# Performance work log

Hardware: AMD Instinct MI355X
Metric: run time of the kernel (lower is better)

The kernel has to match this reference:

```python
import jax, jax.numpy as jnp
import numpy as np

N_PTS, HID, N_LAYERS, N_HEAD, B = 21, 128, 4, 4, 8192
EPS_LN = 1e-6


def _cheb(x, adj, W, b):
    # ChebConv with K=2 (3 orders): T0=I, T1=L, T2=2*L@L - I, L = I - D^-1/2 A D^-1/2
    d = jnp.sum(adj, axis=-1) ** -0.5
    L = jnp.eye(N_PTS, dtype=x.dtype) - d[:, None] * adj * d[None, :]
    t1 = jnp.einsum('ij,bjc->bic', L, x)
    t2 = 2.0 * jnp.einsum('ij,bjc->bic', L, t1) - x
    return (jnp.einsum('bnc,cd->bnd', x, W[0])
            + jnp.einsum('bnc,cd->bnd', t1, W[1])
            + jnp.einsum('bnc,cd->bnd', t2, W[2])) + b


def _layer_norm(x, a, b):
    # matches custom LayerNorm: unbiased std (torch default), eps added to std
    mean = jnp.mean(x, -1, keepdims=True)
    xm = x - mean
    std = jnp.sqrt(jnp.sum(xm * xm, -1, keepdims=True) / (x.shape[-1] - 1))
    return a * xm / (std + EPS_LN) + b


def _mha(x, mask, Wq, bq, Wk, bk, Wv, bv, Wo, bo):
    Bn, N, D = x.shape
    dk = D // N_HEAD
    def proj(W, b):
        return (x @ W + b).reshape(Bn, N, N_HEAD, dk).transpose(0, 2, 1, 3)
    Q, K, V = proj(Wq, bq), proj(Wk, bk), proj(Wv, bv)
    scores = jnp.einsum('bhqd,bhkd->bhqk', Q, K) / np.float32(np.sqrt(dk))
    scores = jnp.where(mask[:, None, :, :], scores, jnp.asarray(-1e9, x.dtype))
    p = jax.nn.softmax(scores, axis=-1)  # dropout is identity at eval
    o = jnp.einsum('bhqk,bhkd->bhqd', p, V).transpose(0, 2, 1, 3).reshape(Bn, N, D)
    return o @ Wo + bo


def _graphnet(x, Ahat, W1, b1, W2, b2):
    # GraphNet feed-forward: two GraphConvs with learnable A_hat
    # laplacian_batch: D from column sums (torch.sum over dim=1), A_hat same per batch
    d = (jnp.sum(Ahat, axis=0) + 1e-5) ** -0.5
    L = d[:, None] * Ahat * d[None, :]
    h = jax.nn.relu(jnp.einsum('ij,bjc->bic', L, x) @ W1 + b1)
    return jnp.einsum('ij,bjc->bic', L, h) @ W2 + b2


def _forward(x, mask, adj, W_in, b_in, W_out, b_out, ln1_a, ln1_b, ln2_a, ln2_b,
             Wq, bq, Wk, bk, Wv, bv, Wo, bo, Ahat, Wg1, bg1, Wg2, bg2,
             Wc1, bc1, Wc2, bc2):
    out = _cheb(x, adj, W_in, b_in)  # [B,21,128]
    for i in range(N_LAYERS):
        # EncoderLayer: pre-norm residual attn, then pre-norm residual GraphNet
        h = _layer_norm(out, ln1_a[i], ln1_b[i])
        out = out + _mha(h, mask, Wq[i], bq[i], Wk[i], bk[i], Wv[i], bv[i], Wo[i], bo[i])
        h = _layer_norm(out, ln2_a[i], ln2_b[i])
        out = out + _graphnet(h, Ahat[i], Wg1[i], bg1[i], Wg2[i], bg2[i])
        # _ResChebGC: residual + relu(cheb(relu(cheb(x))))
        g = jax.nn.relu(_cheb(out, adj, Wc1[i], bc1[i]))
        out = out + jax.nn.relu(_cheb(g, adj, Wc2[i], bc2[i]))
    return _cheb(out, adj, W_out, b_out)  # [B,21,3]


def setup_inputs() -> dict:
    key = jax.random.key(0)
    ks = iter(jax.random.split(key, 40))
    def nrm(shape, s=0.02):
        return jax.random.normal(next(ks), shape, jnp.float32) * s
    L = N_LAYERS
    return dict(
        x=jax.random.normal(next(ks), (B, N_PTS, 2), jnp.float32),
        mask=jnp.ones((1, 1, N_PTS), dtype=bool),
        adj=jax.random.uniform(next(ks), (N_PTS, N_PTS), jnp.float32) + jnp.eye(N_PTS, dtype=jnp.float32),
        W_in=nrm((3, 2, HID), 0.2), b_in=jnp.zeros((HID,), jnp.float32),
        W_out=nrm((3, HID, 3), 0.05), b_out=jnp.zeros((3,), jnp.float32),
        ln1_a=jnp.ones((L, HID), jnp.float32), ln1_b=jnp.zeros((L, HID), jnp.float32),
        ln2_a=jnp.ones((L, HID), jnp.float32), ln2_b=jnp.zeros((L, HID), jnp.float32),
        Wq=nrm((L, HID, HID)), bq=jnp.zeros((L, HID), jnp.float32),
        Wk=nrm((L, HID, HID)), bk=jnp.zeros((L, HID), jnp.float32),
        Wv=nrm((L, HID, HID)), bv=jnp.zeros((L, HID), jnp.float32),
        Wo=nrm((L, HID, HID)), bo=jnp.zeros((L, HID), jnp.float32),
        Ahat=jnp.tile(jnp.eye(N_PTS, dtype=jnp.float32)[None], (L, 1, 1)),
        Wg1=nrm((L, HID, 2 * HID)), bg1=jnp.zeros((L, 2 * HID), jnp.float32),
        Wg2=nrm((L, 2 * HID, HID)), bg2=jnp.zeros((L, HID), jnp.float32),
        Wc1=nrm((L, 3, HID, HID)), bc1=jnp.zeros((L, HID), jnp.float32),
        Wc2=nrm((L, 3, HID, HID)), bc2=jnp.zeros((L, HID), jnp.float32),
    )


def reference(x, mask, adj, W_in, b_in, W_out, b_out, ln1_a, ln1_b, ln2_a, ln2_b,
              Wq, bq, Wk, bk, Wv, bv, Wo, bo, Ahat, Wg1, bg1, Wg2, bg2,
              Wc1, bc1, Wc2, bc2):
    return _forward(x, mask, adj, W_in, b_in, W_out, b_out, ln1_a, ln1_b, ln2_a, ln2_b,
                    Wq, bq, Wk, bk, Wv, bv, Wo, bo, Ahat, Wg1, bg1, Wg2, bg2,
                    Wc1, bc1, Wc2, bc2)
```

## Files before the change

kernel.cpp:

```cpp
#include <hip/hip_runtime.h>

#define DEV static __device__ __forceinline__

typedef __attribute__((ext_vector_type(8))) short short8;
typedef __attribute__((ext_vector_type(4))) short short4v;
typedef __attribute__((ext_vector_type(4))) float f4;

#define OFF_QKV 0
#define OFF_WO  196608
#define OFF_WG1 262144
#define OFF_WG2 393216
#define OFF_WC1 524288
#define OFF_WC2 720896
#define OFF_WIN 917504
#define OFF_WOUT 929792
#define OFF_M1 931840
#define OFF_M2 932864
#define OFF_LG 933888
#define W_TOT  937984

struct WSBuf {
  unsigned short w[W_TOT];
  float m1f[441];
  float m2f[441];
};
__device__ WSBuf g_ws;

DEV float b2f(unsigned short u){ union { unsigned int i; float f; } v; v.i = ((unsigned int)u)<<16; return v.f; }
DEV unsigned short f2b(float f){
  union { float f; unsigned int i; } v; v.f = f;
  unsigned int i = v.i; i += 0x7fffu + ((i>>16)&1u);
  return (unsigned short)(i>>16);
}
DEV f4 mfma(short8 a, short8 b, f4 c){ return __builtin_amdgcn_mfma_f32_16x16x32_bf16(a,b,c,0,0,0); }
DEV f4 mfma16(short4v a, short4v b, f4 c){ return __builtin_amdgcn_mfma_f32_16x16x16bf16_1k(a,b,c,0,0,0); }
DEV short8 ld8(const unsigned short* p){ return *(const short8*)p; }

DEV void st4(unsigned short* p, f4 v){
  short4v o;
  o[0]=(short)f2b(v[0]); o[1]=(short)f2b(v[1]);
  o[2]=(short)f2b(v[2]); o[3]=(short)f2b(v[3]);
  *(short4v*)p = o;
}
DEV void rmw4(unsigned short* p, f4 v){
  short4v x = *(const short4v*)p;
  short4v o;
  o[0]=(short)f2b(b2f((unsigned short)x[0]) + v[0]);
  o[1]=(short)f2b(b2f((unsigned short)x[1]) + v[1]);
  o[2]=(short)f2b(b2f((unsigned short)x[2]) + v[2]);
  o[3]=(short)f2b(b2f((unsigned short)x[3]) + v[3]);
  *(short4v*)p = o;
}
DEV f4 maxz(f4 v){
  v[0]=fmaxf(v[0],0.f); v[1]=fmaxf(v[1],0.f);
  v[2]=fmaxf(v[2],0.f); v[3]=fmaxf(v[3],0.f);
  return v;
}

__global__ void prep_mats(const float* __restrict__ adj,
                          const float* __restrict__ Ahat){
  __shared__ float sA[441], sL[441], sM2[441], sD[21];
  unsigned short* ws = g_ws.w;
  int t = threadIdx.x;
  if (t < 441) sA[t] = adj[t];
  __syncthreads();
  if (t < 21){ float s = 0.f; for (int j=0;j<21;++j) s += sA[t*21+j]; sD[t] = 1.0f/sqrtf(s); }
  __syncthreads();
  if (t < 441){ int i = t/21, j = t%21; sL[t] = ((i==j)?1.f:0.f) - sD[i]*sA[t]*sD[j]; }
  __syncthreads();
  if (t < 441){ int i = t/21, j = t%21; float a=0.f;
    for (int m=0;m<21;++m) a += sL[i*21+m]*sL[m*21+j];
    sM2[t] = 2.f*a - ((i==j)?1.f:0.f); }
  __syncthreads();
  for (int e = t; e < 1024; e += blockDim.x){
    int i = e>>5, j = e&31; bool v = (i<21)&&(j<21);
    ws[OFF_M1+e] = v ? f2b(sL[i*21+j]) : 0;
    ws[OFF_M2+e] = v ? f2b(sM2[i*21+j]) : 0;
  }
  if (t < 441){ g_ws.m1f[t] = sL[t]; g_ws.m2f[t] = sM2[t]; }
  for (int l=0;l<4;++l){
    __syncthreads();
    if (t < 441) sA[t] = Ahat[l*441 + t];
    __syncthreads();
    if (t < 21){ float s = 1e-5f; for (int i=0;i<21;++i) s += sA[i*21+t]; sD[t] = 1.0f/sqrtf(s); }
    __syncthreads();
    for (int e = t; e < 1024; e += blockDim.x){
      int i = e>>5, j = e&31; bool v = (i<21)&&(j<21);
      ws[OFF_LG + l*1024 + e] = v ? f2b(sD[i]*sA[i*21+j]*sD[j]) : 0;
    }
  }
}

__global__ void prep_tw(const float* __restrict__ Wq, const float* __restrict__ Wk,
                        const float* __restrict__ Wv, const float* __restrict__ Wo,
                        const float* __restrict__ Wg1, const float* __restrict__ Wg2,
                        const float* __restrict__ Wc1, const float* __restrict__ Wc2,
                        const float* __restrict__ Win, const float* __restrict__ Wout){
  unsigned short* ws = g_ws.w;
  int stride = gridDim.x*blockDim.x;
  int idx = blockIdx.x*blockDim.x + threadIdx.x;
  for (int e = idx; e < 196608; e += stride){
    int l = e/49152, r = e%49152, n = r>>7, k = r&127;
    int sel = n>>7, c = n&127;
    const float* W = (sel==0)?Wq:((sel==1)?Wk:Wv);
    ws[OFF_QKV+e] = f2b(W[l*16384 + k*128 + c]);
  }
  for (int e = idx; e < 65536; e += stride){
    int l = e>>14, r = e&16383, n = r>>7, k = r&127;
    ws[OFF_WO+e] = f2b(Wo[l*16384 + k*128 + n]);
  }
  for (int e = idx; e < 131072; e += stride){
    int l = e>>15, r = e&32767, n = r>>7, k = r&127;
    ws[OFF_WG1+e] = f2b(Wg1[l*32768 + k*256 + n]);
  }
  for (int e = idx; e < 131072; e += stride){
    int l = e>>15, r = e&32767, n = r>>8, k = r&255;
    ws[OFF_WG2+e] = f2b(Wg2[l*32768 + k*128 + n]);
  }
  for (int e = idx; e < 196608; e += stride){
    int l = e/49152, r = e%49152, n = r>>7, k = r&127;
    int sel = n>>7, c = n&127;
    ws[OFF_WC1+e] = f2b(Wc1[((l*3+sel)*128 + k)*128 + c]);
  }
  for (int e = idx; e < 196608; e += stride){
    int l = e/49152, r = e%49152, n = r>>7, k = r&127;
    int sel = n>>7, c = n&127;
    ws[OFF_WC2+e] = f2b(Wc2[((l*3+sel)*128 + k)*128 + c]);
  }
  for (int e = idx; e < 12288; e += stride){
    int n = e>>5, k = e&31, sel = n>>7, c = n&127;
    ws[OFF_WIN+e] = (k<2) ? f2b(Win[(sel*2 + k)*128 + c]) : 0;
  }
  for (int e = idx; e < 2048; e += stride){
    int n = e>>7, k = e&127;
    ws[OFF_WOUT+e] = (n<9) ? f2b(Wout[((n/3)*128 + k)*3 + (n%3)]) : 0;
  }
}

#define PA 152

template<int MT, int NT, int KS>
DEV void chan_mm(const unsigned short* A, int pitchA,
                 const unsigned short* Bt, int strideB, int n0, int mt0,
                 int lane, f4 acc[MT][NT]){
  const int l16 = lane & 15, qd = lane >> 4;
#pragma unroll
  for (int ks = 0; ks < KS; ++ks){
    const int k0 = ks*32 + qd*8;
    short8 af[MT];
#pragma unroll
    for (int m=0; m<MT; ++m) af[m] = ld8(A + ((mt0+m)*16+l16)*pitchA + k0);
#pragma unroll
    for (int nt=0; nt<NT; ++nt){
      short8 bf = ld8(Bt + (n0 + nt*16 + l16)*strideB + k0);
#pragma unroll
      for (int m=0; m<MT; ++m) acc[m][nt] = mfma(af[m], bf, acc[m][nt]);
    }
  }
}

DEV void node_mm1(const unsigned short* Ut, int mt0,
                  const unsigned short* Mr, int lane, f4 acc[3][2]){
  const int l16 = lane & 15, qd = lane >> 4;
  short8 bf[2];
#pragma unroll
  for (int nt=0; nt<2; ++nt) bf[nt] = ld8(Mr + (nt*16+l16)*32 + qd*8);
#pragma unroll
  for (int b=0;b<3;++b){
    short8 af = ld8(Ut + (mt0*16 + l16)*72 + b*24 + qd*8);
#pragma unroll
    for (int nt=0;nt<2;++nt) acc[b][nt] = mfma(af, bf[nt], acc[b][nt]);
  }
}

template<int KS>
DEV void w0_term1(const unsigned short* Wt0, int sK,
                  const unsigned short* Blds, int pitchB, int mt0,
                  int lane, f4 acc[3][2]){
  const int l16 = lane&15, qd = lane>>4;
#pragma unroll
  for (int ks=0; ks<KS; ++ks){
    const int k0 = ks*32 + qd*8;
    short8 af = ld8(Wt0 + (mt0*16+l16)*sK + k0);
#pragma unroll
    for (int b=0;b<3;++b){
#pragma unroll
      for (int nt=0;nt<2;++nt){
        short8 bf = ld8(Blds + (b*21 + nt*16 + l16)*pitchB + k0);
        acc[b][nt] = mfma(af, bf, acc[b][nt]);
      }
    }
  }
}

DEV void write_tr(unsigned short* Ut, int ch, f4 v, int mt, int qd, float bias, int rmax){
#pragma unroll
  for (int reg=0; reg<4; ++reg){
    int r = mt*16 + qd*4 + reg;
    if (r < rmax){
      int b = (r>=42) ? 2 : ((r>=21)?1:0);
      int n = r - b*21;
      Ut[ch*72 + b*24 + n] = f2b(v[reg] + bias);
    }
  }
}

DEV void layer_norm(const unsigned short* src, unsigned short* dst,
                    const float* ga, const float* gb, int tid){
  int row = tid >> 3, seg = tid & 7;
  const unsigned short* p = src + row*136 + seg*16;
  float xv[16];
#pragma unroll
  for (int j=0;j<2;++j){
    short8 rv = ld8(p + j*8);
#pragma unroll
    for (int i=0;i<8;++i) xv[j*8+i] = b2f((unsigned short)rv[i]);
  }
  float s1=0.f, s2=0.f;
#pragma unroll
  for (int i=0;i<16;++i){ s1 += xv[i]; s2 += xv[i]*xv[i]; }
  s1 += __shfl_xor(s1,1); s2 += __shfl_xor(s2,1);
  s1 += __shfl_xor(s1,2); s2 += __shfl_xor(s2,2);
  s1 += __shfl_xor(s1,4); s2 += __shfl_xor(s2,4);
  float mean = s1 * 0.0078125f;
  float var = (s2 - s1*mean) * (1.0f/127.0f);
  var = fmaxf(var, 0.f);
  float inv = 1.0f/(sqrtf(var) + 1e-6f);
  unsigned short* d = dst + row*PA + seg*16;
#pragma unroll
  for (int j=0;j<2;++j){
    short8 ov;
#pragma unroll
    for (int i=0;i<8;++i){
      float y = ga[seg*16+j*8+i] * (xv[j*8+i]-mean) * inv + gb[seg*16+j*8+i];
      ov[i] = (short)f2b(y);
    }
    *(short8*)(d + j*8) = ov;
  }
}

#define R_RES 0
#define R_A   8704
#define R_TR  18432
#define TRU   9232
#define R_Q   37368
#define R_Y1  47096
#define S_TOT 56824

DEV void cheb_res(const unsigned short* Asrc, int pitchA,
                  const unsigned short* Wcat, const float* bias,
                  bool writeG,
                  unsigned short* s_a, unsigned short* s_tr, unsigned short* s_res,
                  const unsigned short* M1r, const unsigned short* M2r,
                  int lane, int wave, int nb, int rvalid){
  const int l16 = lane&15, qd = lane>>4;
  const f4 z4 = {0.f,0.f,0.f,0.f};
  f4 u1[4], u2[4];
#pragma unroll
  for (int mt=0;mt<4;++mt){ u1[mt]=z4; u2[mt]=z4; }
#pragma unroll
  for (int ks=0;ks<4;++ks){
    const int k0 = ks*32 + qd*8;
    short8 af[4];
#pragma unroll
    for (int m=0;m<4;++m) af[m] = ld8(Asrc + (m*16+l16)*pitchA + k0);
    short8 b1 = ld8(Wcat + (128 + wave*16 + l16)*128 + k0);
    short8 b2 = ld8(Wcat + (256 + wave*16 + l16)*128 + k0);
#pragma unroll
    for (int m=0;m<4;++m){
      u1[m] = mfma(af[m], b1, u1[m]);
      u2[m] = mfma(af[m], b2, u2[m]);
    }
  }
  int ch = wave*16 + l16;
#pragma unroll
  for (int mt=0;mt<4;++mt) write_tr(s_tr,       ch, u1[mt], mt, qd, 0.f, rvalid);
#pragma unroll
  for (int mt=0;mt<4;++mt) write_tr(s_tr + TRU, ch, u2[mt], mt, qd, 0.f, rvalid);
  f4 a2[3][2];
#pragma unroll
  for (int b=0;b<3;++b){ a2[b][0]=z4; a2[b][1]=z4; }
  w0_term1<4>(Wcat, 128, Asrc, pitchA, wave, lane, a2);
  node_mm1(s_tr, wave, M1r, lane, a2);
  node_mm1(s_tr + TRU, wave, M2r, lane, a2);
  const int ch0 = wave*16 + qd*4;
  const f4 vb = *(const f4*)(bias + ch0);
#pragma unroll
  for (int b=0;b<3;++b){ if (b >= nb) continue;
#pragma unroll
    for (int nt=0;nt<2;++nt){
      int o = nt*16 + l16;
      if (o < 21){
        int r = b*21 + o;
        f4 t = maxz(a2[b][nt] + vb);
        if (writeG) st4(&s_a[r*PA + ch0], t);
        else        rmw4(&s_res[r*136 + ch0], t);
      }
    }
  }
  __syncthreads();
}

__launch_bounds__(512, 1)
__global__ void graformer_main(
  const float* __restrict__ x,
  const float* __restrict__ ln1a, const float* __restrict__ ln1b,
  const float* __restrict__ ln2a, const float* __restrict__ ln2b,
  const float* __restrict__ bq, const float* __restrict__ bk,
  const float* __restrict__ bv, const float* __restrict__ bo,
  const float* __restrict__ bg1, const float* __restrict__ bg2,
  const float* __restrict__ bc1, const float* __restrict__ bc2,
  const float* __restrict__ b_in, const float* __restrict__ b_out,
  float* __restrict__ out)
{
  __shared__ __align__(16) unsigned short S[S_TOT];
  unsigned short* s_res = S + R_RES;
  unsigned short* s_a   = S + R_A;
  unsigned short* s_tr  = S + R_TR;
  unsigned short* s_q   = S + R_Q;
  unsigned short* s_y1  = S + R_Y1;
  const unsigned short* ws = g_ws.w;

  const int tid = threadIdx.x;
  const int lane = tid & 63, wave = tid >> 6;
  const int l16 = lane & 15, qd = lane >> 4;
  const int blk = blockIdx.x;
  int nb = 8192 - blk*3; nb = (nb < 3) ? nb : 3;
  const int rvalid = nb*21;
  const f4 z4 = {0.f,0.f,0.f,0.f};
  const unsigned short* M1r = ws + OFF_M1;
  const unsigned short* M2r = ws + OFF_M2;
  const int ch0 = wave*16 + qd*4;

  {
    short8 z8 = {0,0,0,0,0,0,0,0};
    for (int i = tid*8; i < S_TOT; i += 512*8) *(short8*)(S + i) = z8;
  }
  __syncthreads();

  if (tid < 64){
    int r = tid;
    float v0=0.f, v1=0.f;
    if (r < rvalid){
      int b = (r>=42)?2:((r>=21)?1:0);
      int n = r - b*21;
      long g = (long)(blk*3+b)*42 + n*2;
      v0 = x[g]; v1 = x[g+1];
    }
    unsigned short* p = s_a + r*32;
    p[0]=f2b(v0); p[1]=f2b(v1);
#pragma unroll
    for (int k=2;k<32;++k) p[k]=0;
  }
  __syncthreads();

  {
#pragma unroll
    for (int p=1; p<=2; ++p){
      f4 acc[4][1];
#pragma unroll
      for (int mt=0;mt<4;++mt) acc[mt][0]=z4;
      chan_mm<4,1,1>(s_a, 32, ws + OFF_WIN, 32, p*128 + wave*16, 0, lane, acc);
      unsigned short* Ut = (p==1) ? s_tr : (s_tr + TRU);
      int ch = wave*16 + l16;
#pragma unroll
      for (int mt=0;mt<4;++mt) write_tr(Ut, ch, acc[mt][0], mt, qd, 0.f, rvalid);
    }
    f4 a2[3][2];
#pragma unroll
    for (int b=0;b<3;++b){ a2[b][0]=z4; a2[b][1]=z4; }
    w0_term1<1>(ws + OFF_WIN, 32, s_a, 32, wave, lane, a2);
    node_mm1(s_tr, wave, M1r, lane, a2);
    node_mm1(s_tr + TRU, wave, M2r, lane, a2);
    const f4 vbin = *(const f4*)(b_in + ch0);
#pragma unroll
    for (int b=0;b<3;++b){ if (b>=nb) continue;
#pragma unroll
      for (int nt=0;nt<2;++nt){
        int o = nt*16 + l16;
        if (o < 21){ int r = b*21 + o;
          st4(&s_res[r*136 + ch0], a2[b][nt] + vbin);
        }
      }
    }
    __syncthreads();
  }

  for (int l=0; l<4; ++l){
    layer_norm(s_res, s_a, ln1a + l*128, ln1b + l*128, tid);
    __syncthreads();
    {
      {
        f4 ak[4], aq[4];
#pragma unroll
        for (int nt=0;nt<4;++nt){ ak[nt]=z4; aq[nt]=z4; }
        const unsigned short* WK = ws + OFF_QKV + l*49152 + 16384;
        const unsigned short* WQ = ws + OFF_QKV + l*49152;
#pragma unroll
        for (int ks=0;ks<4;++ks){
          const int k0 = ks*32 + qd*8;
          short8 wk = ld8(WK + (wave*16+l16)*128 + k0);
          short8 wq = ld8(WQ + (wave*16+l16)*128 + k0);
#pragma unroll
          for (int nt=0;nt<4;++nt){
            short8 bf = ld8(s_a + (nt*16+l16)*PA + k0);
            ak[nt] = mfma(wk, bf, ak[nt]);
            aq[nt] = mfma(wq, bf, aq[nt]);
          }
        }
        const f4 vbk = *(const f4*)(bk + l*128 + ch0);
        const f4 vbq = *(const f4*)(bq + l*128 + ch0);
#pragma unroll
        for (int nt=0;nt<4;++nt){
          int node = nt*16 + l16;
          st4(&s_tr[node*136 + ch0], ak[nt] + vbk);
          st4(&s_q[node*PA + ch0], aq[nt] + vbq);
        }
      }
      {
        f4 av[2][2]; av[0][0]=z4; av[0][1]=z4; av[1][0]=z4; av[1][1]=z4;
        const int mh2 = (wave>>2)*2, nq = (wave&3)*32;
        chan_mm<2,2,4>(s_a, PA, ws + OFF_QKV + l*49152 + 32768, 128, nq, mh2, lane, av);
#pragma unroll
        for (int nt=0;nt<2;++nt){
          int ch = nq + nt*16 + l16; float bb = bv[l*128+ch];
#pragma unroll
          for (int m=0;m<2;++m) write_tr(s_tr+8704, ch, av[m][nt], mh2+m, qd, bb, rvalid);
        }
      }
      __syncthreads();
    }
    {
#pragma unroll
      for (int i=0;i<3;++i){
        int u = wave + 8*i;
        int pair = u >> 1, mt = u & 1;
        int b = pair>>2, h = pair&3;
        f4 sc[2]; sc[0]=z4; sc[1]=z4;
        short8 qb = ld8(s_q + (b*21 + mt*16 + l16)*PA + h*32 + qd*8);
#pragma unroll
        for (int nt=0;nt<2;++nt){
          short8 ka = ld8(s_tr + (b*21 + nt*16 + l16)*136 + h*32 + qd*8);
          sc[nt] = mfma(ka, qb, sc[nt]);
        }
        const float scale = 0.1767766952966369f;
        float s0[4], s1[4];
        float m = -1e30f;
#pragma unroll
        for (int reg=0;reg<4;++reg){
          s0[reg] = sc[0][reg]*scale;
          bool kv = (16 + qd*4 + reg) < 21;
          s1[reg] = kv ? sc[1][reg]*scale : -1e30f;
          m = fmaxf(m, fmaxf(s0[reg], s1[reg]));
        }
        m = fmaxf(m, __shfl_xor(m,16));
        m = fmaxf(m, __shfl_xor(m,32));
        float e0[4], e1[4];
        float sum = 0.f;
#pragma unroll
        for (int reg=0;reg<4;++reg){
          e0[reg] = __expf(s0[reg]-m);
          e1[reg] = ((16+qd*4+reg)<21) ? __expf(s1[reg]-m) : 0.f;
          sum += e0[reg]+e1[reg];
        }
        sum += __shfl_xor(sum,16);
        sum += __shfl_xor(sum,32);
        float rinv = 1.f/sum;
        if (b < nb){
          short4v pa0, pa1;
#pragma unroll
          for (int reg=0;reg<4;++reg){
            pa0[reg] = (short)f2b(e0[reg]*rinv);
            pa1[reg] = (short)f2b(e1[reg]*rinv);
          }
          f4 oa[2]; oa[0]=z4; oa[1]=z4;
#pragma unroll
          for (int nt=0;nt<2;++nt){
            int ch = h*32 + nt*16 + l16;
            const unsigned short* vp = s_tr + 8704 + ch*72 + b*24;
            short4v vb0 = *(const short4v*)(vp + qd*4);
            short4v vb1 = *(const short4v*)(vp + 16 + qd*4);
            oa[nt] = mfma16(vb0, pa0, oa[nt]);
            oa[nt] = mfma16(vb1, pa1, oa[nt]);
          }
          int q = mt*16 + l16;
          if (q < 21){
            int row = (b*21 + q)*PA + h*32;
#pragma unroll
            for (int nt=0;nt<2;++nt)
              st4(&s_a[row + nt*16 + qd*4], oa[nt]);
          }
        }
      }
      __syncthreads();
    }
    {
      f4 ao[1][4];
#pragma unroll
      for (int nt=0;nt<4;++nt) ao[0][nt]=z4;
      chan_mm<1,4,4>(ws + OFF_WO + l*16384, 128, s_a, PA, 0, wave, lane, ao);
      const f4 vbo = *(const f4*)(bo + l*128 + ch0);
#pragma unroll
      for (int nt=0;nt<4;++nt){
        int node = nt*16 + l16;
        if (node < rvalid)
          rmw4(&s_res[node*136 + ch0], ao[0][nt] + vbo);
      }
      __syncthreads();
    }
    layer_norm(s_res, s_a, ln2a + l*128, ln2b + l*128, tid);
    __syncthreads();
    {
      f4 u1[4], u2[4];
#pragma unroll
      for (int mt=0;mt<4;++mt){ u1[mt]=z4; u2[mt]=z4; }
      {
        const unsigned short* W1 = ws + OFF_WG1 + l*32768;
#pragma unroll
        for (int ks=0;ks<4;++ks){
          const int k0 = ks*32 + qd*8;
          short8 af[4];
#pragma unroll
          for (int m=0;m<4;++m) af[m] = ld8(s_a + (m*16+l16)*PA + k0);
          short8 b1 = ld8(W1 + (wave*16+l16)*128 + k0);
          short8 b2 = ld8(W1 + 16384 + (wave*16+l16)*128 + k0);
#pragma unroll
          for (int m=0;m<4;++m){
            u1[m] = mfma(af[m], b1, u1[m]);
            u2[m] = mfma(af[m], b2, u2[m]);
          }
        }
      }
      int ch = wave*16 + l16;
      {
#pragma unroll
        for (int mt=0;mt<4;++mt) write_tr(s_tr, ch, u1[mt], mt, qd, 0.f, rvalid);
        f4 y[3][2];
#pragma unroll
        for (int b=0;b<3;++b){ y[b][0]=z4; y[b][1]=z4; }
        node_mm1(s_tr, wave, ws + OFF_LG + l*1024, lane, y);
        const f4 vb1 = *(const f4*)(bg1 + l*256 + ch0);
#pragma unroll
        for (int b=0;b<3;++b){ if (b>=nb) continue;
#pragma unroll
          for (int nt=0;nt<2;++nt){
            int o = nt*16+l16;
            if (o<21){ int r = b*21+o;
              st4(&s_tr[TRU + r*PA + ch0], maxz(y[b][nt] + vb1));
            }
          }
        }
      }
      {
#pragma unroll
        for (int mt=0;mt<4;++mt) write_tr(s_tr, ch, u2[mt], mt, qd, 0.f, rvalid);
        f4 y[3][2];
#pragma unroll
        for (int b=0;b<3;++b){ y[b][0]=z4; y[b][1]=z4; }
        node_mm1(s_tr, wave, ws + OFF_LG + l*1024, lane, y);
        const f4 vb1b = *(const f4*)(bg1 + l*256 + 128 + ch0);
#pragma unroll
        for (int b=0;b<3;++b){ if (b>=nb) continue;
#pragma unroll
          for (int nt=0;nt<2;++nt){
            int o = nt*16+l16;
            if (o<21){ int r = b*21+o;
              st4(&s_y1[r*PA + ch0], maxz(y[b][nt] + vb1b));
            }
          }
        }
      }
      __syncthreads();
      f4 Z[4];
#pragma unroll
      for (int mt=0;mt<4;++mt) Z[mt]=z4;
      {
        const unsigned short* W2 = ws + OFF_WG2 + l*32768;
#pragma unroll
        for (int ks=0;ks<4;++ks){
          const int k0 = ks*32 + qd*8;
          short8 a0[4], a1[4];
#pragma unroll
          for (int m=0;m<4;++m) a0[m] = ld8(s_tr + TRU + (m*16+l16)*PA + k0);
#pragma unroll
          for (int m=0;m<4;++m) a1[m] = ld8(s_y1 + (m*16+l16)*PA + k0);
          short8 b0 = ld8(W2 + (wave*16+l16)*256 + k0);
          short8 b1 = ld8(W2 + (wave*16+l16)*256 + 128 + k0);
#pragma unroll
          for (int m=0;m<4;++m){
            Z[m] = mfma(a0[m], b0, Z[m]);
            Z[m] = mfma(a1[m], b1, Z[m]);
          }
        }
      }
      {
#pragma unroll
        for (int mt=0;mt<4;++mt) write_tr(s_tr, ch, Z[mt], mt, qd, 0.f, rvalid);
      }
      f4 fz[3][2];
#pragma unroll
      for (int b=0;b<3;++b){ fz[b][0]=z4; fz[b][1]=z4; }
      node_mm1(s_tr, wave, ws + OFF_LG + l*1024, lane, fz);
      {
        const f4 vb2 = *(const f4*)(bg2 + l*128 + ch0);
#pragma unroll
        for (int b=0;b<3;++b){ if (b>=nb) continue;
#pragma unroll
          for (int nt=0;nt<2;++nt){
            int o = nt*16+l16;
            if (o<21){ int r = b*21+o;
              rmw4(&s_res[r*136 + ch0], fz[b][nt] + vb2);
            }
          }
        }
      }
      __syncthreads();
    }
    cheb_res(s_res, 136, ws + OFF_WC1 + l*49152, bc1 + l*128, true,
             s_a, s_tr, s_res, M1r, M2r, lane, wave, nb, rvalid);
    cheb_res(s_a, PA, ws + OFF_WC2 + l*49152, bc2 + l*128, false,
             s_a, s_tr, s_res, M1r, M2r, lane, wave, nb, rvalid);
  }

  {
    f4 acc = z4;
    if (wave < 4){
#pragma unroll
      for (int ks=0;ks<4;++ks){
        int k0 = ks*32 + qd*8;
        short8 af = ld8(s_res + (wave*16 + l16)*136 + k0);
        short8 bf = ld8(ws + OFF_WOUT + l16*128 + k0);
        acc = mfma(af, bf, acc);
      }
    }
    float* sf = (float*)s_a;
    if (wave < 4 && l16 < 9){
#pragma unroll
      for (int reg=0;reg<4;++reg){
        int r = wave*16 + qd*4 + reg;
        if (r < 63) sf[r*12 + l16] = acc[reg];
      }
    }
    __syncthreads();
    if (tid < 189){
      int r = tid/3, c = tid - r*3;
      int b = (r>=42)?2:((r>=21)?1:0);
      int n = r - b*21;
      if (b < nb){
        const float* M1f = g_ws.m1f;
        const float* M2f = g_ws.m2f;
        float a = sf[r*12 + c] + b_out[c];
        for (int m=0;m<21;++m){
          a += M1f[n*21+m]*sf[(b*21+m)*12 + 3 + c];
          a += M2f[n*21+m]*sf[(b*21+m)*12 + 6 + c];
        }
        out[((long)(blk*3+b)*21 + n)*3 + c] = a;
      }
    }
  }
}

extern "C" void kernel_launch(void* const* d_in, const int* in_sizes, int n_in,
                              void* d_out, int out_size, void* d_ws, size_t ws_size,
                              hipStream_t stream){
  const float* x    = (const float*)d_in[0];
  const float* adj  = (const float*)d_in[2];
  const float* Win  = (const float*)d_in[3];
  const float* b_in = (const float*)d_in[4];
  const float* Wout = (const float*)d_in[5];
  const float* b_out= (const float*)d_in[6];
  const float* ln1a = (const float*)d_in[7];
  const float* ln1b = (const float*)d_in[8];
  const float* ln2a = (const float*)d_in[9];
  const float* ln2b = (const float*)d_in[10];
  const float* Wq = (const float*)d_in[11];
  const float* bq = (const float*)d_in[12];
  const float* Wk = (const float*)d_in[13];
  const float* bk = (const float*)d_in[14];
  const float* Wv = (const float*)d_in[15];
  const float* bv = (const float*)d_in[16];
  const float* Wo = (const float*)d_in[17];
  const float* bo = (const float*)d_in[18];
  const float* Ahat = (const float*)d_in[19];
  const float* Wg1 = (const float*)d_in[20];
  const float* bg1 = (const float*)d_in[21];
  const float* Wg2 = (const float*)d_in[22];
  const float* bg2 = (const float*)d_in[23];
  const float* Wc1 = (const float*)d_in[24];
  const float* bc1 = (const float*)d_in[25];
  const float* Wc2 = (const float*)d_in[26];
  const float* bc2 = (const float*)d_in[27];
  float* outp = (float*)d_out;

  hipLaunchKernelGGL(prep_mats, dim3(1), dim3(512), 0, stream, adj, Ahat);
  hipLaunchKernelGGL(prep_tw, dim3(512), dim3(256), 0, stream,
                     Wq, Wk, Wv, Wo, Wg1, Wg2, Wc1, Wc2, Win, Wout);
  hipLaunchKernelGGL(graformer_main, dim3(2731), dim3(512), 0, stream,
                     x, ln1a, ln1b, ln2a, ln2b, bq, bk, bv, bo,
                     bg1, bg2, bc1, bc2, b_in, b_out, outp);
}
```

Baseline: 1.352 ms.

## Halve block to 256 threads with two column passes per wave, shrink LDS

Each block now runs 4 waves instead of 8. Every wave handles two 16-channel tiles in sequence, and launch bounds become (256,2). Dedicated Q and Y1 LDS buffers are dropped by reusing s_a, with an extra barrier added, so LDS per block shrinks enough for two blocks per CU. The input ChebConv is folded into the templated cheb_res. The aim is more resident blocks to hide latency, at the cost of per-block serialization and register pressure from holding Q accumulators across the K pass.

```diff
diff --git a/kernel.cpp b/kernel.cpp
--- a/kernel.cpp
+++ b/kernel.cpp
@@ -207,32 +207,31 @@
 
 DEV void layer_norm(const unsigned short* src, unsigned short* dst,
                     const float* ga, const float* gb, int tid){
-  int row = tid >> 3, seg = tid & 7;
-  const unsigned short* p = src + row*136 + seg*16;
-  float xv[16];
-#pragma unroll
-  for (int j=0;j<2;++j){
+  int row = tid >> 2, seg = tid & 3;
+  const unsigned short* p = src + row*136 + seg*32;
+  float xv[32];
+#pragma unroll
+  for (int j=0;j<4;++j){
     short8 rv = ld8(p + j*8);
 #pragma unroll
     for (int i=0;i<8;++i) xv[j*8+i] = b2f((unsigned short)rv[i]);
   }
   float s1=0.f, s2=0.f;
 #pragma unroll
-  for (int i=0;i<16;++i){ s1 += xv[i]; s2 += xv[i]*xv[i]; }
+  for (int i=0;i<32;++i){ s1 += xv[i]; s2 += xv[i]*xv[i]; }
   s1 += __shfl_xor(s1,1); s2 += __shfl_xor(s2,1);
   s1 += __shfl_xor(s1,2); s2 += __shfl_xor(s2,2);
-  s1 += __shfl_xor(s1,4); s2 += __shfl_xor(s2,4);
   float mean = s1 * 0.0078125f;
   float var = (s2 - s1*mean) * (1.0f/127.0f);
   var = fmaxf(var, 0.f);
   float inv = 1.0f/(sqrtf(var) + 1e-6f);
-  unsigned short* d = dst + row*PA + seg*16;
-#pragma unroll
-  for (int j=0;j<2;++j){
+  unsigned short* d = dst + row*PA + seg*32;
+#pragma unroll
+  for (int j=0;j<4;++j){
     short8 ov;
 #pragma unroll
     for (int i=0;i<8;++i){
-      float y = ga[seg*16+j*8+i] * (xv[j*8+i]-mean) * inv + gb[seg*16+j*8+i];
+      float y = ga[seg*32+j*8+i] * (xv[j*8+i]-mean) * inv + gb[seg*32+j*8+i];
       ov[i] = (short)f2b(y);
     }
     *(short8*)(d + j*8) = ov;
@@ -243,65 +242,73 @@
 #define R_A   8704
 #define R_TR  18432
 #define TRU   9232
-#define R_Q   37368
-#define R_Y1  47096
-#define S_TOT 56824
-
+#define S_TOT 37368
+
+template<int KS, int SK>
 DEV void cheb_res(const unsigned short* Asrc, int pitchA,
-                  const unsigned short* Wcat, const float* bias,
-                  bool writeG,
+                  const unsigned short* Wcat, const float* bias, int mode,
                   unsigned short* s_a, unsigned short* s_tr, unsigned short* s_res,
                   const unsigned short* M1r, const unsigned short* M2r,
                   int lane, int wave, int nb, int rvalid){
   const int l16 = lane&15, qd = lane>>4;
   const f4 z4 = {0.f,0.f,0.f,0.f};
-  f4 u1[4], u2[4];
-#pragma unroll
-  for (int mt=0;mt<4;++mt){ u1[mt]=z4; u2[mt]=z4; }
-#pragma unroll
-  for (int ks=0;ks<4;++ks){
-    const int k0 = ks*32 + qd*8;
-    short8 af[4];
-#pragma unroll
-    for (int m=0;m<4;++m) af[m] = ld8(Asrc + (m*16+l16)*pitchA + k0);
-    short8 b1 = ld8(Wcat + (128 + wave*16 + l16)*128 + k0);
-    short8 b2 = ld8(Wcat + (256 + wave*16 + l16)*128 + k0);
-#pragma unroll
-    for (int m=0;m<4;++m){
-      u1[m] = mfma(af[m], b1, u1[m]);
-      u2[m] = mfma(af[m], b2, u2[m]);
-    }
-  }
-  int ch = wave*16 + l16;
-#pragma unroll
-  for (int mt=0;mt<4;++mt) write_tr(s_tr,       ch, u1[mt], mt, qd, 0.f, rvalid);
-#pragma unroll
-  for (int mt=0;mt<4;++mt) write_tr(s_tr + TRU, ch, u2[mt], mt, qd, 0.f, rvalid);
-  f4 a2[3][2];
-#pragma unroll
-  for (int b=0;b<3;++b){ a2[b][0]=z4; a2[b][1]=z4; }
-  w0_term1<4>(Wcat, 128, Asrc, pitchA, wave, lane, a2);
-  node_mm1(s_tr, wave, M1r, lane, a2);
-  node_mm1(s_tr + TRU, wave, M2r, lane, a2);
-  const int ch0 = wave*16 + qd*4;
-  const f4 vb = *(const f4*)(bias + ch0);
-#pragma unroll
-  for (int b=0;b<3;++b){ if (b >= nb) continue;
-#pragma unroll
-    for (int nt=0;nt<2;++nt){
-      int o = nt*16 + l16;
-      if (o < 21){
-        int r = b*21 + o;
-        f4 t = maxz(a2[b][nt] + vb);
-        if (writeG) st4(&s_a[r*PA + ch0], t);
-        else        rmw4(&s_res[r*136 + ch0], t);
+#pragma unroll
+  for (int h2=0; h2<2; ++h2){
+    const int rt = wave + 4*h2;
+    f4 u1[4], u2[4];
+#pragma unroll
+    for (int mt=0;mt<4;++mt){ u1[mt]=z4; u2[mt]=z4; }
+    const unsigned short* W1p = Wcat + (128 + rt*16 + l16)*SK;
+    const unsigned short* W2p = Wcat + (256 + rt*16 + l16)*SK;
+#pragma unroll
+    for (int ks=0;ks<KS;++ks){
+      const int k0 = ks*32 + qd*8;
+      short8 af[4];
+#pragma unroll
+      for (int m=0;m<4;++m) af[m] = ld8(Asrc + (m*16+l16)*pitchA + k0);
+      short8 b1 = ld8(W1p + k0);
+      short8 b2 = ld8(W2p + k0);
+#pragma unroll
+      for (int m=0;m<4;++m){
+        u1[m] = mfma(af[m], b1, u1[m]);
+        u2[m] = mfma(af[m], b2, u2[m]);
+      }
+    }
+    int ch = rt*16 + l16;
+#pragma unroll
+    for (int mt=0;mt<4;++mt) write_tr(s_tr,       ch, u1[mt], mt, qd, 0.f, rvalid);
+#pragma unroll
+    for (int mt=0;mt<4;++mt) write_tr(s_tr + TRU, ch, u2[mt], mt, qd, 0.f, rvalid);
+  }
+#pragma unroll
+  for (int h2=0; h2<2; ++h2){
+    const int rt = wave + 4*h2;
+    f4 a2[3][2];
+#pragma unroll
+    for (int b=0;b<3;++b){ a2[b][0]=z4; a2[b][1]=z4; }
+    w0_term1<KS>(Wcat, SK, Asrc, pitchA, rt, lane, a2);
+    node_mm1(s_tr, rt, M1r, lane, a2);
+    node_mm1(s_tr + TRU, rt, M2r, lane, a2);
+    const int ch0h = rt*16 + qd*4;
+    const f4 vb = *(const f4*)(bias + ch0h);
+#pragma unroll
+    for (int b=0;b<3;++b){ if (b >= nb) continue;
+#pragma unroll
+      for (int nt=0;nt<2;++nt){
+        int o = nt*16 + l16;
+        if (o < 21){
+          int r = b*21 + o;
+          if (mode == 0)      st4(&s_a[r*PA + ch0h], maxz(a2[b][nt] + vb));
+          else if (mode == 1) rmw4(&s_res[r*136 + ch0h], maxz(a2[b][nt] + vb));
+          else                st4(&s_res[r*136 + ch0h], a2[b][nt] + vb);
+        }
       }
     }
   }
   __syncthreads();
 }
 
-__launch_bounds__(512, 1)
+__launch_bounds__(256, 2)
 __global__ void graformer_main(
   const float* __restrict__ x,
   const float* __restrict__ ln1a, const float* __restrict__ ln1b,
@@ -317,8 +324,6 @@
   unsigned short* s_res = S + R_RES;
   unsigned short* s_a   = S + R_A;
   unsigned short* s_tr  = S + R_TR;
-  unsigned short* s_q   = S + R_Q;
-  unsigned short* s_y1  = S + R_Y1;
   const unsigned short* ws = g_ws.w;
 
   const int tid = threadIdx.x;
@@ -330,11 +335,10 @@
   const f4 z4 = {0.f,0.f,0.f,0.f};
   const unsigned short* M1r = ws + OFF_M1;
   const unsigned short* M2r = ws + OFF_M2;
-  const int ch0 = wave*16 + qd*4;
 
   {
     short8 z8 = {0,0,0,0,0,0,0,0};
-    for (int i = tid*8; i < S_TOT; i += 512*8) *(short8*)(S + i) = z8;
+    for (int i = tid*8; i < S_TOT; i += 256*8) *(short8*)(S + i) = z8;
   }
   __syncthreads();
 
@@ -354,90 +358,75 @@
   }
   __syncthreads();
 
-  {
-#pragma unroll
-    for (int p=1; p<=2; ++p){
-      f4 acc[4][1];
-#pragma unroll
-      for (int mt=0;mt<4;++mt) acc[mt][0]=z4;
-      chan_mm<4,1,1>(s_a, 32, ws + OFF_WIN, 32, p*128 + wave*16, 0, lane, acc);
-      unsigned short* Ut = (p==1) ? s_tr : (s_tr + TRU);
-      int ch = wave*16 + l16;
-#pragma unroll
-      for (int mt=0;mt<4;++mt) write_tr(Ut, ch, acc[mt][0], mt, qd, 0.f, rvalid);
-    }
-    f4 a2[3][2];
-#pragma unroll
-    for (int b=0;b<3;++b){ a2[b][0]=z4; a2[b][1]=z4; }
-    w0_term1<1>(ws + OFF_WIN, 32, s_a, 32, wave, lane, a2);
-    node_mm1(s_tr, wave, M1r, lane, a2);
-    node_mm1(s_tr + TRU, wave, M2r, lane, a2);
-    const f4 vbin = *(const f4*)(b_in + ch0);
-#pragma unroll
-    for (int b=0;b<3;++b){ if (b>=nb) continue;
-#pragma unroll
-      for (int nt=0;nt<2;++nt){
-        int o = nt*16 + l16;
-        if (o < 21){ int r = b*21 + o;
-          st4(&s_res[r*136 + ch0], a2[b][nt] + vbin);
-        }
-      }
-    }
-    __syncthreads();
-  }
+  cheb_res<1,32>(s_a, 32, ws + OFF_WIN, b_in, 2,
+                 s_a, s_tr, s_res, M1r, M2r, lane, wave, nb, rvalid);
 
   for (int l=0; l<4; ++l){
     layer_norm(s_res, s_a, ln1a + l*128, ln1b + l*128, tid);
     __syncthreads();
     {
-      {
-        f4 ak[4], aq[4];
-#pragma unroll
-        for (int nt=0;nt<4;++nt){ ak[nt]=z4; aq[nt]=z4; }
-        const unsigned short* WK = ws + OFF_QKV + l*49152 + 16384;
-        const unsigned short* WQ = ws + OFF_QKV + l*49152;
+      f4 aq2[2][4];
+#pragma unroll
+      for (int h2=0; h2<2; ++h2){
+        const int rt = wave + 4*h2;
+        f4 ak[4];
+#pragma unroll
+        for (int nt=0;nt<4;++nt){ ak[nt]=z4; aq2[h2][nt]=z4; }
+        const unsigned short* WK = ws + OFF_QKV + l*49152 + 16384 + (rt*16+l16)*128;
+        const unsigned short* WQ = ws + OFF_QKV + l*49152 + (rt*16+l16)*128;
 #pragma unroll
         for (int ks=0;ks<4;++ks){
           const int k0 = ks*32 + qd*8;
-          short8 wk = ld8(WK + (wave*16+l16)*128 + k0);
-          short8 wq = ld8(WQ + (wave*16+l16)*128 + k0);
+          short8 wk = ld8(WK + k0);
+          short8 wq = ld8(WQ + k0);
 #pragma unroll
           for (int nt=0;nt<4;++nt){
             short8 bf = ld8(s_a + (nt*16+l16)*PA + k0);
             ak[nt] = mfma(wk, bf, ak[nt]);
-            aq[nt] = mfma(wq, bf, aq[nt]);
-          }
-        }
-        const f4 vbk = *(const f4*)(bk + l*128 + ch0);
-        const f4 vbq = *(const f4*)(bq + l*128 + ch0);
-#pragma unroll
-        for (int nt=0;nt<4;++nt){
-          int node = nt*16 + l16;
-          st4(&s_tr[node*136 + ch0], ak[nt] + vbk);
-          st4(&s_q[node*PA + ch0], aq[nt] + vbq);
-        }
+            aq2[h2][nt] = mfma(wq, bf, aq2[h2][nt]);
+          }
+        }
+        const int ch0h = rt*16 + qd*4;
+        const f4 vbk = *(const f4*)(bk + l*128 + ch0h);
+#pragma unroll
+        for (int nt=0;nt<4;++nt)
+          st4(&s_tr[(nt*16+l16)*136 + ch0h], ak[nt] + vbk);
       }
       {
-        f4 av[2][2]; av[0][0]=z4; av[0][1]=z4; av[1][0]=z4; av[1][1]=z4;
-        const int mh2 = (wave>>2)*2, nq = (wave&3)*32;
-        chan_mm<2,2,4>(s_a, PA, ws + OFF_QKV + l*49152 + 32768, 128, nq, mh2, lane, av);
-#pragma unroll
-        for (int nt=0;nt<2;++nt){
-          int ch = nq + nt*16 + l16; float bb = bv[l*128+ch];
-#pragma unroll
-          for (int m=0;m<2;++m) write_tr(s_tr+8704, ch, av[m][nt], mh2+m, qd, bb, rvalid);
+        const int mh2 = (wave>>1)*2;
+#pragma unroll
+        for (int h2=0; h2<2; ++h2){
+          const int nqv = (wave&1)*64 + h2*32;
+          f4 av[2][2]; av[0][0]=z4; av[0][1]=z4; av[1][0]=z4; av[1][1]=z4;
+          chan_mm<2,2,4>(s_a, PA, ws + OFF_QKV + l*49152 + 32768, 128, nqv, mh2, lane, av);
+#pragma unroll
+          for (int nt=0;nt<2;++nt){
+            int ch = nqv + nt*16 + l16; float bb = bv[l*128+ch];
+#pragma unroll
+            for (int m=0;m<2;++m) write_tr(s_tr+8704, ch, av[m][nt], mh2+m, qd, bb, rvalid);
+          }
         }
       }
       __syncthreads();
+#pragma unroll
+      for (int h2=0; h2<2; ++h2){
+        const int rt = wave + 4*h2;
+        const int ch0h = rt*16 + qd*4;
+        const f4 vbq = *(const f4*)(bq + l*128 + ch0h);
+#pragma unroll
+        for (int nt=0;nt<4;++nt)
+          st4(&s_a[(nt*16+l16)*PA + ch0h], aq2[h2][nt] + vbq);
+      }
+      __syncthreads();
     }
     {
 #pragma unroll
-      for (int i=0;i<3;++i){
-        int u = wave + 8*i;
+      for (int i=0;i<6;++i){
+        int u = wave + 4*i;
         int pair = u >> 1, mt = u & 1;
         int b = pair>>2, h = pair&3;
         f4 sc[2]; sc[0]=z4; sc[1]=z4;
-        short8 qb = ld8(s_q + (b*21 + mt*16 + l16)*PA + h*32 + qd*8);
+        short8 qb = ld8(s_a + (b*21 + mt*16 + l16)*PA + h*32 + qd*8);
 #pragma unroll
         for (int nt=0;nt<2;++nt){
           short8 ka = ld8(s_tr + (b*21 + nt*16 + l16)*136 + h*32 + qd*8);
@@ -495,87 +484,99 @@
       __syncthreads();
     }
     {
-      f4 ao[1][4];
-#pragma unroll
-      for (int nt=0;nt<4;++nt) ao[0][nt]=z4;
-      chan_mm<1,4,4>(ws + OFF_WO + l*16384, 128, s_a, PA, 0, wave, lane, ao);
-      const f4 vbo = *(const f4*)(bo + l*128 + ch0);
-#pragma unroll
-      for (int nt=0;nt<4;++nt){
-        int node = nt*16 + l16;
-        if (node < rvalid)
-          rmw4(&s_res[node*136 + ch0], ao[0][nt] + vbo);
+#pragma unroll
+      for (int h2=0; h2<2; ++h2){
+        const int rt = wave + 4*h2;
+        f4 ao[1][4];
+#pragma unroll
+        for (int nt=0;nt<4;++nt) ao[0][nt]=z4;
+        chan_mm<1,4,4>(ws + OFF_WO + l*16384, 128, s_a, PA, 0, rt, lane, ao);
+        const int ch0h = rt*16 + qd*4;
+        const f4 vbo = *(const f4*)(bo + l*128 + ch0h);
+#pragma unroll
+        for (int nt=0;nt<4;++nt){
+          int node = nt*16 + l16;
+          if (node < rvalid)
+            rmw4(&s_res[node*136 + ch0h], ao[0][nt] + vbo);
+        }
       }
       __syncthreads();
     }
     layer_norm(s_res, s_a, ln2a + l*128, ln2b + l*128, tid);
     __syncthreads();
     {
-      f4 u1[4], u2[4];
-#pragma unroll
-      for (int mt=0;mt<4;++mt){ u1[mt]=z4; u2[mt]=z4; }
-      {
-        const unsigned short* W1 = ws + OFF_WG1 + l*32768;
+#pragma unroll
+      for (int h2=0; h2<2; ++h2){
+        const int rt = wave + 4*h2;
+        f4 u1[4], u2[4];
+#pragma unroll
+        for (int mt=0;mt<4;++mt){ u1[mt]=z4; u2[mt]=z4; }
+        const unsigned short* W1 = ws + OFF_WG1 + l*32768 + (rt*16+l16)*128;
 #pragma unroll
         for (int ks=0;ks<4;++ks){
           const int k0 = ks*32 + qd*8;
           short8 af[4];
 #pragma unroll
           for (int m=0;m<4;++m) af[m] = ld8(s_a + (m*16+l16)*PA + k0);
-          short8 b1 = ld8(W1 + (wave*16+l16)*128 + k0);
-          short8 b2 = ld8(W1 + 16384 + (wave*16+l16)*128 + k0);
+          short8 b1 = ld8(W1 + k0);
+          short8 b2 = ld8(W1 + 16384 + k0);
 #pragma unroll
           for (int m=0;m<4;++m){
             u1[m] = mfma(af[m], b1, u1[m]);
             u2[m] = mfma(af[m], b2, u2[m]);
           }
         }
-      }
-      int ch = wave*16 + l16;
-      {
+        const int ch = rt*16 + l16;
 #pragma unroll
         for (int mt=0;mt<4;++mt) write_tr(s_tr, ch, u1[mt], mt, qd, 0.f, rvalid);
         f4 y[3][2];
 #pragma unroll
         for (int b=0;b<3;++b){ y[b][0]=z4; y[b][1]=z4; }
-        node_mm1(s_tr, wave, ws + OFF_LG + l*1024, lane, y);
-        const f4 vb1 = *(const f4*)(bg1 + l*256 + ch0);
+        node_mm1(s_tr, rt, ws + OFF_LG + l*1024, lane, y);
+        const int ch0h = rt*16 + qd*4;
+        const f4 vb1 = *(const f4*)(bg1 + l*256 + ch0h);
 #pragma unroll
         for (int b=0;b<3;++b){ if (b>=nb) continue;
 #pragma unroll
           for (int nt=0;nt<2;++nt){
             int o = nt*16+l16;
             if (o<21){ int r = b*21+o;
-              st4(&s_tr[TRU + r*PA + ch0], maxz(y[b][nt] + vb1));
+              st4(&s_tr[TRU + r*PA + ch0h], maxz(y[b][nt] + vb1));
             }
           }
         }
-      }
-      {
 #pragma unroll
         for (int mt=0;mt<4;++mt) write_tr(s_tr, ch, u2[mt], mt, qd, 0.f, rvalid);
+      }
+      __syncthreads();
+#pragma unroll
+      for (int h2=0; h2<2; ++h2){
+        const int rt = wave + 4*h2;
         f4 y[3][2];
 #pragma unroll
         for (int b=0;b<3;++b){ y[b][0]=z4; y[b][1]=z4; }
-        node_mm1(s_tr, wave, ws + OFF_LG + l*1024, lane, y);
-        const f4 vb1b = *(const f4*)(bg1 + l*256 + 128 + ch0);
+        node_mm1(s_tr, rt, ws + OFF_LG + l*1024, lane, y);
+        const int ch0h = rt*16 + qd*4;
+        const f4 vb1b = *(const f4*)(bg1 + l*256 + 128 + ch0h);
 #pragma unroll
         for (int b=0;b<3;++b){ if (b>=nb) continue;
 #pragma unroll
           for (int nt=0;nt<2;++nt){
             int o = nt*16+l16;
             if (o<21){ int r = b*21+o;
-              st4(&s_y1[r*PA + ch0], maxz(y[b][nt] + vb1b));
+              st4(&s_a[r*PA + ch0h], maxz(y[b][nt] + vb1b));
             }
           }
         }
       }
       __syncthreads();
-      f4 Z[4];
-#pragma unroll
-      for (int mt=0;mt<4;++mt) Z[mt]=z4;
-      {
-        const unsigned short* W2 = ws + OFF_WG2 + l*32768;
+#pragma unroll
+      for (int h2=0; h2<2; ++h2){
+        const int rt = wave + 4*h2;
+        f4 Z[4];
+#pragma unroll
+        for (int mt=0;mt<4;++mt) Z[mt]=z4;
+        const unsigned short* W2 = ws + OFF_WG2 + l*32768 + (rt*16+l16)*256;
 #pragma unroll
         for (int ks=0;ks<4;++ks){
           const int k0 = ks*32 + qd*8;
@@ -583,48 +584,46 @@
 #pragma unroll
           for (int m=0;m<4;++m) a0[m] = ld8(s_tr + TRU + (m*16+l16)*PA + k0);
 #pragma unroll
-          for (int m=0;m<4;++m) a1[m] = ld8(s_y1 + (m*16+l16)*PA + k0);
-          short8 b0 = ld8(W2 + (wave*16+l16)*256 + k0);
-          short8 b1 = ld8(W2 + (wave*16+l16)*256 + 128 + k0);
+          for (int m=0;m<4;++m) a1[m] = ld8(s_a + (m*16+l16)*PA + k0);
+          short8 b0 = ld8(W2 + k0);
+          short8 b1 = ld8(W2 + 128 + k0);
 #pragma unroll
           for (int m=0;m<4;++m){
             Z[m] = mfma(a0[m], b0, Z[m]);
             Z[m] = mfma(a1[m], b1, Z[m]);
           }
         }
-      }
-      {
+        const int ch = rt*16 + l16;
 #pragma unroll
         for (int mt=0;mt<4;++mt) write_tr(s_tr, ch, Z[mt], mt, qd, 0.f, rvalid);
-      }
-      f4 fz[3][2];
-#pragma unroll
-      for (int b=0;b<3;++b){ fz[b][0]=z4; fz[b][1]=z4; }
-      node_mm1(s_tr, wave, ws + OFF_LG + l*1024, lane, fz);
-      {
-        const f4 vb2 = *(const f4*)(bg2 + l*128 + ch0);
+        f4 fz[3][2];
+#pragma unroll
+        for (int b=0;b<3;++b){ fz[b][0]=z4; fz[b][1]=z4; }
+        node_mm1(s_tr, rt, ws + OFF_LG + l*1024, lane, fz);
+        const int ch0h = rt*16 + qd*4;
+        const f4 vb2 = *(const f4*)(bg2 + l*128 + ch0h);
 #pragma unroll
         for (int b=0;b<3;++b){ if (b>=nb) continue;
 #pragma unroll
           for (int nt=0;nt<2;++nt){
             int o = nt*16+l16;
             if (o<21){ int r = b*21+o;
-              rmw4(&s_res[r*136 + ch0], fz[b][nt] + vb2);
+              rmw4(&s_res[r*136 + ch0h], fz[b][nt] + vb2);
             }
           }
         }
       }
       __syncthreads();
     }
-    cheb_res(s_res, 136, ws + OFF_WC1 + l*49152, bc1 + l*128, true,
-             s_a, s_tr, s_res, M1r, M2r, lane, wave, nb, rvalid);
-    cheb_res(s_a, PA, ws + OFF_WC2 + l*49152, bc2 + l*128, false,
-             s_a, s_tr, s_res, M1r, M2r, lane, wave, nb, rvalid);
+    cheb_res<4,128>(s_res, 136, ws + OFF_WC1 + l*49152, bc1 + l*128, 0,
+                    s_a, s_tr, s_res, M1r, M2r, lane, wave, nb, rvalid);
+    cheb_res<4,128>(s_a, PA, ws + OFF_WC2 + l*49152, bc2 + l*128, 1,
+                    s_a, s_tr, s_res, M1r, M2r, lane, wave, nb, rvalid);
   }
 
   {
     f4 acc = z4;
-    if (wave < 4){
+    {
 #pragma unroll
       for (int ks=0;ks<4;++ks){
         int k0 = ks*32 + qd*8;
@@ -634,7 +633,7 @@
       }
     }
     float* sf = (float*)s_a;
-    if (wave < 4 && l16 < 9){
+    if (l16 < 9){
 #pragma unroll
       for (int reg=0;reg<4;++reg){
         int r = wave*16 + qd*4 + reg;
@@ -695,7 +694,7 @@
   hipLaunchKernelGGL(prep_mats, dim3(1), dim3(512), 0, stream, adj, Ahat);
   hipLaunchKernelGGL(prep_tw, dim3(512), dim3(256), 0, stream,
                      Wq, Wk, Wv, Wo, Wg1, Wg2, Wc1, Wc2, Win, Wout);
-  hipLaunchKernelGGL(graformer_main, dim3(2731), dim3(512), 0, stream,
+  hipLaunchKernelGGL(graformer_main, dim3(2731), dim3(256), 0, stream,
                      x, ln1a, ln1b, ln2a, ln2b, bq, bk, bv, bo,
                      bg1, bg2, bc1, bc2, b_in, b_out, outp);
 }
```

Result: slower. 1.716 ms (+27.0%).
